# Kernel tuning notes

Hardware: AMD Instinct MI355X
Metric: run time of the kernel (lower is better)

## Reference

```python
import jax, jax.numpy as jnp
import numpy as np

SEQ_LEN = 200
BATCH = 32768
H = 4  # LSTM hidden size


def _lstm_layer(x, Wih, Whh, bih, bhh):
    """PyTorch-semantics LSTM layer. x: [B,T,D] -> [B,T,H]. Gate order i,f,g,o."""
    # precompute input contribution for all timesteps: [B,T,4H]
    xg = jnp.einsum('btd,gd->btg', x, Wih) + bih + bhh

    def step(carry, xt):
        h, c = carry
        g = xt + h @ Whh.T  # [B,4H]
        i, f, gg, o = jnp.split(g, 4, axis=-1)
        c = jax.nn.sigmoid(f) * c + jax.nn.sigmoid(i) * jnp.tanh(gg)
        h = jax.nn.sigmoid(o) * jnp.tanh(c)
        return (h, c), h

    B = x.shape[0]
    z = jnp.zeros((B, Whh.shape[1]), x.dtype)
    _, hs = jax.lax.scan(step, (z, z), jnp.swapaxes(xg, 0, 1))  # [T,B,H]
    return jnp.swapaxes(hs, 0, 1)


def _lstm2(x, Wih0, Whh0, bih0, bhh0, Wih1, Whh1, bih1, bhh1):
    h = _lstm_layer(x, Wih0, Whh0, bih0, bhh0)
    return _lstm_layer(h, Wih1, Whh1, bih1, bhh1)


def setup_inputs() -> dict:
    key = jax.random.key(0)
    ks = iter(jax.random.split(key, 64))
    def p(shape, s=0.1):
        return jax.random.normal(next(ks), shape, jnp.float32) * s
    d = {"x": jax.random.normal(next(ks), (BATCH, 2, SEQ_LEN), jnp.float32)}
    for r in ("r0", "r1"):
        d[f"{r}_Wih0"] = p((4 * H, 1)); d[f"{r}_Whh0"] = p((4 * H, H))
        d[f"{r}_bih0"] = p((4 * H,));  d[f"{r}_bhh0"] = p((4 * H,))
        d[f"{r}_Wih1"] = p((4 * H, H)); d[f"{r}_Whh1"] = p((4 * H, H))
        d[f"{r}_bih1"] = p((4 * H,));  d[f"{r}_bhh1"] = p((4 * H,))
    d["Wp"] = p((40, 2 * SEQ_LEN)); d["bp"] = p((40,))
    d["WH"] = p((128, 4 * SEQ_LEN)); d["bH"] = p((128,))
    d["WL"] = p((128, 4 * SEQ_LEN)); d["bL"] = p((128,))
    d["W1"] = p((80, 256)); d["b1"] = p((80,))
    d["W2"] = p((40, 80)); d["b2"] = p((40,))
    d["W3"] = p((1, 80)); d["b3"] = p((1,))
    return d


def reference(x,
              r0_Wih0, r0_Whh0, r0_bih0, r0_bhh0, r0_Wih1, r0_Whh1, r0_bih1, r0_bhh1,
              r1_Wih0, r1_Whh0, r1_bih0, r1_bhh0, r1_Wih1, r1_Whh1, r1_bih1, r1_bhh1,
              Wp, bp, WH, bH, WL, bL, W1, b1, W2, b2, W3, b3):
    B = x.shape[0]
    x_flat = x.reshape(B, 2 * SEQ_LEN)
    other = x_flat @ Wp.T + bp  # [B,40]

    Hx = x[:, 0, :, None]  # [B,T,1]
    Lx = x[:, 1, :, None]
    Hh = _lstm2(Hx, r0_Wih0, r0_Whh0, r0_bih0, r0_bhh0, r0_Wih1, r0_Whh1, r0_bih1, r0_bhh1)
    Lh = _lstm2(Lx, r1_Wih0, r1_Whh0, r1_bih0, r1_bhh0, r1_Wih1, r1_Whh1, r1_bih1, r1_bhh1)
    Hf = jnp.tanh(Hh.reshape(B, 4 * SEQ_LEN) @ WH.T + bH)  # [B,128]
    Lf = jnp.tanh(Lh.reshape(B, 4 * SEQ_LEN) @ WL.T + bL)
    z = jnp.concatenate([Hf, Lf], axis=1)  # [B,256]
    z = jnp.tanh(z @ W1.T + b1)  # [B,80]
    z = jnp.tanh(z @ W2.T + b2)  # [B,40]
    z = jnp.concatenate([z, other], axis=1)  # [B,80]
    return jax.nn.sigmoid(z @ W3.T + b3)  # [B,1]
```

## Files before the change

### kernel.cpp

```cpp
#include <hip/hip_runtime.h>
#include <hip/hip_bf16.h>

#define BATCH 32768
#define TSEQ 200

typedef __attribute__((ext_vector_type(8))) short short8;
typedef __attribute__((ext_vector_type(4))) float floatx4;
typedef __attribute__((ext_vector_type(2))) float f32x2;

#if __has_builtin(__builtin_amdgcn_exp2f)
__device__ __forceinline__ float EXP2(float x) { return __builtin_amdgcn_exp2f(x); }
#else
__device__ __forceinline__ float EXP2(float x) {
    float r; asm("v_exp_f32 %0, %1" : "=v"(r) : "v"(x)); return r;
}
#endif

__device__ __forceinline__ float fast_sigmoid(float x) {
    return __builtin_amdgcn_rcpf(1.0f + EXP2(-1.4426950408889634f * x));
}
__device__ __forceinline__ float fast_tanh(float x) {
    float e = EXP2(2.8853900817779268f * x);
    return 1.0f - 2.0f * __builtin_amdgcn_rcpf(e + 1.0f);
}
__device__ __forceinline__ short f2bfs(float v) {
    __hip_bfloat16 h = __float2bfloat16(v);
    return __builtin_bit_cast(short, h);
}
__device__ __forceinline__ f32x2 splat2(float x) { f32x2 v; v[0] = x; v[1] = x; return v; }
__device__ __forceinline__ f32x2 pkfma(f32x2 a, f32x2 b, f32x2 c) {
    return __builtin_elementwise_fma(a, b, c);
}
template <int K>
__device__ __forceinline__ float qb(float v) {
    int i = __builtin_bit_cast(int, v);
    int r = __builtin_amdgcn_update_dpp(i, i, K * 0x55, 0xf, 0xf, false);
    return __builtin_bit_cast(float, r);
}
__device__ __forceinline__ void rcp4(float d0, float d1, float d2, float d3,
                                     float& i0, float& i1, float& i2, float& i3) {
    float p01 = d0 * d1, p23 = d2 * d3;
    float r = __builtin_amdgcn_rcpf(p01 * p23);
    float r01 = r * p23, r23 = r * p01;
    i0 = r01 * d1; i1 = r01 * d0; i2 = r23 * d3; i3 = r23 * d2;
}
__device__ __forceinline__ void async16(void* lds, const void* g) {
    __builtin_amdgcn_global_load_lds(
        (const __attribute__((address_space(1))) unsigned int*)g,
        (__attribute__((address_space(3))) unsigned int*)lds, 16, 0, 0);
}

#define S_SIG (-1.4426950408889634f)
#define S_TANH (2.8853900817779268f)

#define WS_HH  0
#define WS_WHB 104857600
#define WS_WLB (WS_WHB + 204800)
#define WS_W1B (WS_WLB + 204800)
#define WS_W2B (WS_W1B + 40960)
#define WS_U   (WS_W2B + 9216)
#define WS_OT  (WS_U + 1616)
#define WS_Z   (WS_OT + 262144)

struct LW { const float* p[16]; };

__global__ __launch_bounds__(256) void k_prep(
    const float* __restrict__ WH, const float* __restrict__ WL,
    const float* __restrict__ W1, const float* __restrict__ W2,
    const float* __restrict__ W3, const float* __restrict__ Wp,
    const float* __restrict__ bp, const float* __restrict__ b3,
    __hip_bfloat16* __restrict__ WHbf, __hip_bfloat16* __restrict__ WLbf,
    __hip_bfloat16* __restrict__ W1bf, __hip_bfloat16* __restrict__ W2bf,
    float* __restrict__ u)
{
    int gid = blockIdx.x * 256 + threadIdx.x;
    int n = gid / 800, k = gid - n * 800;
    int t = k >> 2, q = k & 3;
    int kp = (t >> 2) * 16 + q * 4 + (t & 3);
    int dst = n * 800 + kp;
    WHbf[dst] = __float2bfloat16(WH[gid]);
    WLbf[dst] = __float2bfloat16(WL[gid]);
    if (gid < 20480) W1bf[gid] = __float2bfloat16(W1[gid]);
    if (gid < 4608) {
        int rr = gid / 96, cc = gid - rr * 96;
        float v = (rr < 40 && cc < 80) ? W2[rr * 80 + cc] : 0.0f;
        W2bf[gid] = __float2bfloat16(v);
    }
    if (gid < 400) {
        float a = 0.f;
        for (int j = 0; j < 40; ++j) a = fmaf(W3[40 + j], Wp[j * 400 + gid], a);
        u[gid] = a;
    } else if (gid == 400) {
        float a = b3[0];
        for (int j = 0; j < 40; ++j) a = fmaf(W3[40 + j], bp[j], a);
        u[400] = a;
    }
}

__global__ __launch_bounds__(256, 4) void k_lstm(
    const float* __restrict__ x, LW w, const float* __restrict__ u,
    __hip_bfloat16* __restrict__ hh, float* __restrict__ otherp)
{
    int gid = blockIdx.x * 256 + threadIdx.x;
    int q = gid & 3;
    int group = gid >> 2;
    int b = group & (BATCH - 1);
    int r = group >> 15;

    const float* Wih0 = w.p[r * 8 + 0];
    const float* Whh0 = w.p[r * 8 + 1];
    const float* bih0 = w.p[r * 8 + 2];
    const float* bhh0 = w.p[r * 8 + 3];
    const float* Wih1 = w.p[r * 8 + 4];
    const float* Whh1 = w.p[r * 8 + 5];
    const float* bih1 = w.p[r * 8 + 6];
    const float* bhh1 = w.p[r * 8 + 7];

    f32x2 wx0p[2], bb0p[2], bb1p[2], whh0p[2][4], wih1p[2][4], whh1p[2][4];
#pragma unroll
    for (int p = 0; p < 2; ++p) {
#pragma unroll
        for (int c = 0; c < 2; ++c) {
            int G = 2 * p + c;
            int j = 4 * G + q;
            float sc = (G == 2) ? S_TANH : S_SIG;
            wx0p[p][c] = Wih0[j] * sc;
            bb0p[p][c] = (bih0[j] + bhh0[j]) * sc;
            bb1p[p][c] = (bih1[j] + bhh1[j]) * sc;
#pragma unroll
            for (int k = 0; k < 4; ++k) {
                whh0p[p][k][c] = Whh0[j * 4 + k] * sc;
                wih1p[p][k][c] = Wih1[j * 4 + k] * sc;
                whh1p[p][k][c] = Whh1[j * 4 + k] * sc;
            }
        }
    }

    const float* xp = x + ((size_t)b * 2 + r) * TSEQ;
    const float* up = u + r * TSEQ;
    __hip_bfloat16* hp = hh + ((size_t)r * BATCH + b) * 800 + q * 4;

    float h0 = 0.f, c0 = 0.f, h1 = 0.f, c1 = 0.f, accO = 0.f;

    for (int tb = 0; tb < TSEQ; tb += 4) {
        float4 xv = *(const float4*)(xp + tb);
        float4 uv = *(const float4*)(up + tb);
        float xa[4] = {xv.x, xv.y, xv.z, xv.w};
        float ua[4] = {uv.x, uv.y, uv.z, uv.w};
        float hb[4];
#pragma unroll
        for (int j = 0; j < 4; ++j) {
            float xt = xa[j];
            accO = fmaf(xt, ua[j], accO);

            float a0 = qb<0>(h0), a1 = qb<1>(h0), a2 = qb<2>(h0), a3 = qb<3>(h0);
            f32x2 g0 = pkfma(splat2(xt), wx0p[0], bb0p[0]);
            f32x2 g1 = pkfma(splat2(xt), wx0p[1], bb0p[1]);
            g0 = pkfma(whh0p[0][0], splat2(a0), g0); g1 = pkfma(whh0p[1][0], splat2(a0), g1);
            g0 = pkfma(whh0p[0][1], splat2(a1), g0); g1 = pkfma(whh0p[1][1], splat2(a1), g1);
            g0 = pkfma(whh0p[0][2], splat2(a2), g0); g1 = pkfma(whh0p[1][2], splat2(a2), g1);
            g0 = pkfma(whh0p[0][3], splat2(a3), g0); g1 = pkfma(whh0p[1][3], splat2(a3), g1);
            float di = 1.0f + EXP2(g0[0]);
            float df = 1.0f + EXP2(g0[1]);
            float dt = 1.0f + EXP2(g1[0]);
            float dn = 1.0f + EXP2(g1[1]);
            float ig, fg, it_, og;
            rcp4(di, df, dt, dn, ig, fg, it_, og);
            float tg = fmaf(-2.0f, it_, 1.0f);
            c0 = fmaf(fg, c0, ig * tg);
            float dc0 = 1.0f + EXP2(S_TANH * c0);
            float th0 = fmaf(-2.0f, __builtin_amdgcn_rcpf(dc0), 1.0f);
            h0 = og * th0;

            float p0 = qb<0>(h0), p1 = qb<1>(h0), p2 = qb<2>(h0), p3 = qb<3>(h0);
            float q0 = qb<0>(h1), q1 = qb<1>(h1), q2 = qb<2>(h1), q3 = qb<3>(h1);
            g0 = bb1p[0]; g1 = bb1p[1];
            g0 = pkfma(wih1p[0][0], splat2(p0), g0); g1 = pkfma(wih1p[1][0], splat2(p0), g1);
            g0 = pkfma(wih1p[0][1], splat2(p1), g0); g1 = pkfma(wih1p[1][1], splat2(p1), g1);
            g0 = pkfma(wih1p[0][2], splat2(p2), g0); g1 = pkfma(wih1p[1][2], splat2(p2), g1);
            g0 = pkfma(wih1p[0][3], splat2(p3), g0); g1 = pkfma(wih1p[1][3], splat2(p3), g1);
            g0 = pkfma(whh1p[0][0], splat2(q0), g0); g1 = pkfma(whh1p[1][0], splat2(q0), g1);
            g0 = pkfma(whh1p[0][1], splat2(q1), g0); g1 = pkfma(whh1p[1][1], splat2(q1), g1);
            g0 = pkfma(whh1p[0][2], splat2(q2), g0); g1 = pkfma(whh1p[1][2], splat2(q2), g1);
            g0 = pkfma(whh1p[0][3], splat2(q3), g0); g1 = pkfma(whh1p[1][3], splat2(q3), g1);
            di = 1.0f + EXP2(g0[0]);
            df = 1.0f + EXP2(g0[1]);
            dt = 1.0f + EXP2(g1[0]);
            dn = 1.0f + EXP2(g1[1]);
            rcp4(di, df, dt, dn, ig, fg, it_, og);
            tg = fmaf(-2.0f, it_, 1.0f);
            c1 = fmaf(fg, c1, ig * tg);
            float dc1 = 1.0f + EXP2(S_TANH * c1);
            float th1 = fmaf(-2.0f, __builtin_amdgcn_rcpf(dc1), 1.0f);
            h1 = og * th1;
            hb[j] = h1;
        }
        ushort4 pk;
        pk.x = (unsigned short)f2bfs(hb[0]);
        pk.y = (unsigned short)f2bfs(hb[1]);
        pk.z = (unsigned short)f2bfs(hb[2]);
        pk.w = (unsigned short)f2bfs(hb[3]);
        *(ushort4*)(hp + tb * 4) = pk;
    }
    if (q == 0) otherp[(size_t)r * BATCH + b] = accO;
}

__global__ __launch_bounds__(256) void k_gemm(
    const __hip_bfloat16* __restrict__ hh,
    const __hip_bfloat16* __restrict__ WHbf, const __hip_bfloat16* __restrict__ WLbf,
    const float* __restrict__ bH, const float* __restrict__ bL,
    __hip_bfloat16* __restrict__ zws)
{
    __shared__ __hip_bfloat16 As[2][128 * 32];
    __shared__ __hip_bfloat16 Bs[2][128 * 32];
    int tid = threadIdx.x;
    int f = blockIdx.y;
    int m0 = blockIdx.x * 128;
    const __hip_bfloat16* A = hh + (size_t)f * BATCH * 800 + (size_t)m0 * 800;
    const __hip_bfloat16* Wb = f ? WLbf : WHbf;
    const float* bias = f ? bL : bH;

    int wv = tid >> 6, lane = tid & 63, l15 = lane & 15, quad = lane >> 4;
    const __hip_bfloat16* ga = A + (size_t)(tid >> 2) * 800 + (tid & 3) * 8;
    const __hip_bfloat16* gb = Wb + (size_t)(tid >> 2) * 800 + (tid & 3) * 8;

    floatx4 acc[2][8] = {};

#define PREFETCH(kc, buf)                                              \
    do {                                                               \
        __hip_bfloat16* la = &As[buf][wv * 512];                       \
        __hip_bfloat16* lb = &Bs[buf][wv * 512];                       \
        async16(la,        ga + (kc) * 32);                            \
        async16(lb,        gb + (kc) * 32);                            \
        async16(la + 2048, ga + 64 * 800 + (kc) * 32);                 \
        async16(lb + 2048, gb + 64 * 800 + (kc) * 32);                 \
    } while (0)

    PREFETCH(0, 0);
    for (int kc = 0; kc < 25; ++kc) {
        __syncthreads();
        if (kc < 24) PREFETCH(kc + 1, (kc + 1) & 1);
        int buf = kc & 1;
        short8 af0 = *(const short8*)(const void*)&As[buf][(wv * 32 + l15) * 32 + quad * 8];
        short8 af1 = *(const short8*)(const void*)&As[buf][(wv * 32 + 16 + l15) * 32 + quad * 8];
#pragma unroll
        for (int nt = 0; nt < 8; ++nt) {
            short8 bfr = *(const short8*)(const void*)&Bs[buf][(nt * 16 + l15) * 32 + quad * 8];
            acc[0][nt] = __builtin_amdgcn_mfma_f32_16x16x32_bf16(af0, bfr, acc[0][nt], 0, 0, 0);
            acc[1][nt] = __builtin_amdgcn_mfma_f32_16x16x32_bf16(af1, bfr, acc[1][nt], 0, 0, 0);
        }
    }
#undef PREFETCH

    float bv[8];
#pragma unroll
    for (int nt = 0; nt < 8; ++nt) bv[nt] = bias[nt * 16 + l15];
#pragma unroll
    for (int mt = 0; mt < 2; ++mt)
#pragma unroll
        for (int nt = 0; nt < 8; ++nt)
#pragma unroll
            for (int rg = 0; rg < 4; ++rg) {
                int row = m0 + wv * 32 + mt * 16 + quad * 4 + rg;
                int col = f * 128 + nt * 16 + l15;
                zws[(size_t)row * 256 + col] =
                    __float2bfloat16(fast_tanh(acc[mt][nt][rg] + bv[nt]));
            }
}

__global__ __launch_bounds__(256) void k_tail(
    const __hip_bfloat16* __restrict__ zws,
    const __hip_bfloat16* __restrict__ W1bf, const __hip_bfloat16* __restrict__ W2bf,
    const float* __restrict__ b1, const float* __restrict__ b2,
    const float* __restrict__ W3, const float* __restrict__ u,
    const float* __restrict__ otherp, float* __restrict__ out)
{
    __shared__ short z1sh[64 * 104];
    __shared__ float z2sh[64 * 49];
    int tid = threadIdx.x;
    int wv = tid >> 6, lane = tid & 63, l15 = lane & 15, quad = lane >> 4;
    int m0 = blockIdx.x * 64;

    for (int i = tid; i < 64 * 24; i += 256) {
        int rr = i / 24, cc = 80 + (i - rr * 24);
        z1sh[rr * 104 + cc] = 0;
    }

    {
        floatx4 acc[5] = {};
#pragma unroll
        for (int kc = 0; kc < 8; ++kc) {
            short8 af = *(const short8*)(const void*)
                (zws + (size_t)(m0 + wv * 16 + l15) * 256 + kc * 32 + quad * 8);
#pragma unroll
            for (int nt = 0; nt < 5; ++nt) {
                short8 bfr = *(const short8*)(const void*)
                    (W1bf + (size_t)(nt * 16 + l15) * 256 + kc * 32 + quad * 8);
                acc[nt] = __builtin_amdgcn_mfma_f32_16x16x32_bf16(af, bfr, acc[nt], 0, 0, 0);
            }
        }
#pragma unroll
        for (int nt = 0; nt < 5; ++nt) {
            int n = nt * 16 + l15;
            float bb = b1[n];
#pragma unroll
            for (int rg = 0; rg < 4; ++rg) {
                int ml = wv * 16 + quad * 4 + rg;
                z1sh[ml * 104 + n] = f2bfs(fast_tanh(acc[nt][rg] + bb));
            }
        }
    }
    __syncthreads();

    {
        floatx4 acc[3] = {};
#pragma unroll
        for (int kc = 0; kc < 3; ++kc) {
            short8 af = *(const short8*)(const void*)
                &z1sh[(wv * 16 + l15) * 104 + kc * 32 + quad * 8];
#pragma unroll
            for (int nt = 0; nt < 3; ++nt) {
                short8 bfr = *(const short8*)(const void*)
                    (W2bf + (size_t)(nt * 16 + l15) * 96 + kc * 32 + quad * 8);
                acc[nt] = __builtin_amdgcn_mfma_f32_16x16x32_bf16(af, bfr, acc[nt], 0, 0, 0);
            }
        }
#pragma unroll
        for (int nt = 0; nt < 3; ++nt) {
            int n = nt * 16 + l15;
            if (n < 40) {
                float bb = b2[n];
#pragma unroll
                for (int rg = 0; rg < 4; ++rg) {
                    int ml = wv * 16 + quad * 4 + rg;
                    z2sh[ml * 49 + n] = fast_tanh(acc[nt][rg] + bb);
                }
            }
        }
    }
    __syncthreads();

    if (tid < 64) {
        int grow = m0 + tid;
        float s = u[400] + otherp[grow] + otherp[BATCH + grow];
        for (int j = 0; j < 40; ++j) s = fmaf(z2sh[tid * 49 + j], W3[j], s);
        out[grow] = fast_sigmoid(s);
    }
}

extern "C" void kernel_launch(void* const* d_in, const int* in_sizes, int n_in,
                              void* d_out, int out_size, void* d_ws, size_t ws_size,
                              hipStream_t stream)
{
    const float* x = (const float*)d_in[0];
    LW w;
    for (int i = 0; i < 16; ++i) w.p[i] = (const float*)d_in[1 + i];
    const float* Wp = (const float*)d_in[17];
    const float* bp = (const float*)d_in[18];
    const float* WH = (const float*)d_in[19];
    const float* bH = (const float*)d_in[20];
    const float* WL = (const float*)d_in[21];
    const float* bL = (const float*)d_in[22];
    const float* W1 = (const float*)d_in[23];
    const float* b1 = (const float*)d_in[24];
    const float* W2 = (const float*)d_in[25];
    const float* b2 = (const float*)d_in[26];
    const float* W3 = (const float*)d_in[27];
    const float* b3 = (const float*)d_in[28];

    char* ws = (char*)d_ws;
    __hip_bfloat16* hh   = (__hip_bfloat16*)(ws + WS_HH);
    __hip_bfloat16* WHbf = (__hip_bfloat16*)(ws + WS_WHB);
    __hip_bfloat16* WLbf = (__hip_bfloat16*)(ws + WS_WLB);
    __hip_bfloat16* W1bf = (__hip_bfloat16*)(ws + WS_W1B);
    __hip_bfloat16* W2bf = (__hip_bfloat16*)(ws + WS_W2B);
    float* u      = (float*)(ws + WS_U);
    float* otherp = (float*)(ws + WS_OT);
    __hip_bfloat16* zws = (__hip_bfloat16*)(ws + WS_Z);
    float* out = (float*)d_out;

    k_prep<<<400, 256, 0, stream>>>(WH, WL, W1, W2, W3, Wp, bp, b3,
                                    WHbf, WLbf, W1bf, W2bf, u);
    k_lstm<<<1024, 256, 0, stream>>>(x, w, u, hh, otherp);
    k_gemm<<<dim3(256, 2), 256, 0, stream>>>(hh, WHbf, WLbf, bH, bL, zws);
    k_tail<<<512, 256, 0, stream>>>(zws, W1bf, W2bf, b1, b2, W3, u, otherp, out);
}
```

Baseline: 349.6 us.

## Fuse head GEMM into tail MLP kernel and pin LSTM weights in registers

The separate WH/WL projection GEMM kernel is merged into the tail kernel. Each 64-row block now computes both 128-wide feature halves into shared memory and runs the W1/W2/W3 MLP directly, with no round trip of the z activations through global memory and one fewer launch. The cost is a smaller M tile per block, so weight tiles are reused less and WH/WL are reloaded more often. The LSTM kernel also switches to an explicit waves_per_eu attribute and uses empty asm constraints to keep its weights resident in VGPRs.

Result: no change. 356.1 us (+1.8%).

```diff
diff --git a/kernel.cpp b/kernel.cpp
--- a/kernel.cpp
+++ b/kernel.cpp
@@ -31,6 +31,7 @@
 __device__ __forceinline__ f32x2 pkfma(f32x2 a, f32x2 b, f32x2 c) {
     return __builtin_elementwise_fma(a, b, c);
 }
+__device__ __forceinline__ void pin2(f32x2& v) { asm volatile("" : "+v"(v)); }
 template <int K>
 __device__ __forceinline__ float qb(float v) {
     int i = __builtin_bit_cast(int, v);
@@ -60,7 +61,6 @@
 #define WS_W2B (WS_W1B + 40960)
 #define WS_U   (WS_W2B + 9216)
 #define WS_OT  (WS_U + 1616)
-#define WS_Z   (WS_OT + 262144)
 
 struct LW { const float* p[16]; };
 
@@ -97,7 +97,8 @@
     }
 }
 
-__global__ __launch_bounds__(256, 4) void k_lstm(
+__global__ __launch_bounds__(256)
+__attribute__((amdgpu_waves_per_eu(4, 4))) void k_lstm(
     const float* __restrict__ x, LW w, const float* __restrict__ u,
     __hip_bfloat16* __restrict__ hh, float* __restrict__ otherp)
 {
@@ -133,6 +134,14 @@
                 wih1p[p][k][c] = Wih1[j * 4 + k] * sc;
                 whh1p[p][k][c] = Whh1[j * 4 + k] * sc;
             }
+        }
+    }
+#pragma unroll
+    for (int p = 0; p < 2; ++p) {
+        pin2(wx0p[p]); pin2(bb0p[p]); pin2(bb1p[p]);
+#pragma unroll
+        for (int k = 0; k < 4; ++k) {
+            pin2(whh0p[p][k]); pin2(wih1p[p][k]); pin2(whh1p[p][k]);
         }
     }
 
@@ -205,98 +214,92 @@
     if (q == 0) otherp[(size_t)r * BATCH + b] = accO;
 }
 
-__global__ __launch_bounds__(256) void k_gemm(
+__global__ __launch_bounds__(256) void k_head(
     const __hip_bfloat16* __restrict__ hh,
     const __hip_bfloat16* __restrict__ WHbf, const __hip_bfloat16* __restrict__ WLbf,
     const float* __restrict__ bH, const float* __restrict__ bL,
-    __hip_bfloat16* __restrict__ zws)
-{
-    __shared__ __hip_bfloat16 As[2][128 * 32];
-    __shared__ __hip_bfloat16 Bs[2][128 * 32];
-    int tid = threadIdx.x;
-    int f = blockIdx.y;
-    int m0 = blockIdx.x * 128;
-    const __hip_bfloat16* A = hh + (size_t)f * BATCH * 800 + (size_t)m0 * 800;
-    const __hip_bfloat16* Wb = f ? WLbf : WHbf;
-    const float* bias = f ? bL : bH;
-
-    int wv = tid >> 6, lane = tid & 63, l15 = lane & 15, quad = lane >> 4;
-    const __hip_bfloat16* ga = A + (size_t)(tid >> 2) * 800 + (tid & 3) * 8;
-    const __hip_bfloat16* gb = Wb + (size_t)(tid >> 2) * 800 + (tid & 3) * 8;
-
-    floatx4 acc[2][8] = {};
-
-#define PREFETCH(kc, buf)                                              \
-    do {                                                               \
-        __hip_bfloat16* la = &As[buf][wv * 512];                       \
-        __hip_bfloat16* lb = &Bs[buf][wv * 512];                       \
-        async16(la,        ga + (kc) * 32);                            \
-        async16(lb,        gb + (kc) * 32);                            \
-        async16(la + 2048, ga + 64 * 800 + (kc) * 32);                 \
-        async16(lb + 2048, gb + 64 * 800 + (kc) * 32);                 \
-    } while (0)
-
-    PREFETCH(0, 0);
-    for (int kc = 0; kc < 25; ++kc) {
-        __syncthreads();
-        if (kc < 24) PREFETCH(kc + 1, (kc + 1) & 1);
-        int buf = kc & 1;
-        short8 af0 = *(const short8*)(const void*)&As[buf][(wv * 32 + l15) * 32 + quad * 8];
-        short8 af1 = *(const short8*)(const void*)&As[buf][(wv * 32 + 16 + l15) * 32 + quad * 8];
-#pragma unroll
-        for (int nt = 0; nt < 8; ++nt) {
-            short8 bfr = *(const short8*)(const void*)&Bs[buf][(nt * 16 + l15) * 32 + quad * 8];
-            acc[0][nt] = __builtin_amdgcn_mfma_f32_16x16x32_bf16(af0, bfr, acc[0][nt], 0, 0, 0);
-            acc[1][nt] = __builtin_amdgcn_mfma_f32_16x16x32_bf16(af1, bfr, acc[1][nt], 0, 0, 0);
-        }
-    }
-#undef PREFETCH
-
-    float bv[8];
-#pragma unroll
-    for (int nt = 0; nt < 8; ++nt) bv[nt] = bias[nt * 16 + l15];
-#pragma unroll
-    for (int mt = 0; mt < 2; ++mt)
-#pragma unroll
-        for (int nt = 0; nt < 8; ++nt)
-#pragma unroll
-            for (int rg = 0; rg < 4; ++rg) {
-                int row = m0 + wv * 32 + mt * 16 + quad * 4 + rg;
-                int col = f * 128 + nt * 16 + l15;
-                zws[(size_t)row * 256 + col] =
-                    __float2bfloat16(fast_tanh(acc[mt][nt][rg] + bv[nt]));
-            }
-}
-
-__global__ __launch_bounds__(256) void k_tail(
-    const __hip_bfloat16* __restrict__ zws,
     const __hip_bfloat16* __restrict__ W1bf, const __hip_bfloat16* __restrict__ W2bf,
     const float* __restrict__ b1, const float* __restrict__ b2,
     const float* __restrict__ W3, const float* __restrict__ u,
     const float* __restrict__ otherp, float* __restrict__ out)
 {
-    __shared__ short z1sh[64 * 104];
-    __shared__ float z2sh[64 * 49];
+    __shared__ short zsh[64 * 264];
+    __shared__ __align__(16) char pool[25856];
+    __hip_bfloat16* As = (__hip_bfloat16*)pool;
+    __hip_bfloat16* Bs = (__hip_bfloat16*)(pool + 8192);
+    short* z1sh = (short*)pool;
+    float* z2sh = (float*)(pool + 13312);
+
     int tid = threadIdx.x;
     int wv = tid >> 6, lane = tid & 63, l15 = lane & 15, quad = lane >> 4;
     int m0 = blockIdx.x * 64;
 
+    int arow = tid >> 2, aseg = tid & 3;
+
+    floatx4 acc[8];
+
+    for (int f = 0; f < 2; ++f) {
+        const __hip_bfloat16* A = hh + ((size_t)f * BATCH + m0) * 800;
+        const __hip_bfloat16* Wb = f ? WLbf : WHbf;
+        const float* bias = f ? bL : bH;
+        const __hip_bfloat16* ga = A + (size_t)arow * 800 + aseg * 8;
+        const __hip_bfloat16* gb = Wb + (size_t)(arow + wv * 16) * 800 + aseg * 8;
+
+#define PREFETCH(kc, buf)                                               \
+    do {                                                                \
+        async16(&As[(buf) * 2048 + wv * 512], ga + (kc) * 32);          \
+        async16(&Bs[(buf) * 4096 + wv * 1024], gb + (kc) * 32);         \
+        async16(&Bs[(buf) * 4096 + wv * 1024 + 512],                    \
+                gb + 16 * 800 + (kc) * 32);                             \
+    } while (0)
+
+        if (f == 1) __syncthreads();
+#pragma unroll
+        for (int nt = 0; nt < 8; ++nt) acc[nt] = (floatx4){0.f, 0.f, 0.f, 0.f};
+        PREFETCH(0, 0);
+        for (int kc = 0; kc < 25; ++kc) {
+            __syncthreads();
+            if (kc < 24) PREFETCH(kc + 1, (kc + 1) & 1);
+            int buf = kc & 1;
+            short8 af = *(const short8*)(const void*)
+                &As[buf * 2048 + (wv * 16 + l15) * 32 + quad * 8];
+#pragma unroll
+            for (int nt = 0; nt < 8; ++nt) {
+                short8 bfr = *(const short8*)(const void*)
+                    &Bs[buf * 4096 + (nt * 16 + l15) * 32 + quad * 8];
+                acc[nt] = __builtin_amdgcn_mfma_f32_16x16x32_bf16(af, bfr, acc[nt], 0, 0, 0);
+            }
+        }
+#undef PREFETCH
+#pragma unroll
+        for (int nt = 0; nt < 8; ++nt) {
+            int n = nt * 16 + l15;
+            float bb = bias[n];
+#pragma unroll
+            for (int rg = 0; rg < 4; ++rg) {
+                int ml = wv * 16 + quad * 4 + rg;
+                zsh[ml * 264 + f * 128 + n] = f2bfs(fast_tanh(acc[nt][rg] + bb));
+            }
+        }
+    }
+    __syncthreads();
+
     for (int i = tid; i < 64 * 24; i += 256) {
         int rr = i / 24, cc = 80 + (i - rr * 24);
         z1sh[rr * 104 + cc] = 0;
     }
 
     {
-        floatx4 acc[5] = {};
+        floatx4 acc1[5] = {};
 #pragma unroll
         for (int kc = 0; kc < 8; ++kc) {
             short8 af = *(const short8*)(const void*)
-                (zws + (size_t)(m0 + wv * 16 + l15) * 256 + kc * 32 + quad * 8);
+                &zsh[(wv * 16 + l15) * 264 + kc * 32 + quad * 8];
 #pragma unroll
             for (int nt = 0; nt < 5; ++nt) {
                 short8 bfr = *(const short8*)(const void*)
                     (W1bf + (size_t)(nt * 16 + l15) * 256 + kc * 32 + quad * 8);
-                acc[nt] = __builtin_amdgcn_mfma_f32_16x16x32_bf16(af, bfr, acc[nt], 0, 0, 0);
+                acc1[nt] = __builtin_amdgcn_mfma_f32_16x16x32_bf16(af, bfr, acc1[nt], 0, 0, 0);
             }
         }
 #pragma unroll
@@ -306,14 +309,14 @@
 #pragma unroll
             for (int rg = 0; rg < 4; ++rg) {
                 int ml = wv * 16 + quad * 4 + rg;
-                z1sh[ml * 104 + n] = f2bfs(fast_tanh(acc[nt][rg] + bb));
+                z1sh[ml * 104 + n] = f2bfs(fast_tanh(acc1[nt][rg] + bb));
             }
         }
     }
     __syncthreads();
 
     {
-        floatx4 acc[3] = {};
+        floatx4 acc2[3] = {};
 #pragma unroll
         for (int kc = 0; kc < 3; ++kc) {
             short8 af = *(const short8*)(const void*)
@@ -322,7 +325,7 @@
             for (int nt = 0; nt < 3; ++nt) {
                 short8 bfr = *(const short8*)(const void*)
                     (W2bf + (size_t)(nt * 16 + l15) * 96 + kc * 32 + quad * 8);
-                acc[nt] = __builtin_amdgcn_mfma_f32_16x16x32_bf16(af, bfr, acc[nt], 0, 0, 0);
+                acc2[nt] = __builtin_amdgcn_mfma_f32_16x16x32_bf16(af, bfr, acc2[nt], 0, 0, 0);
             }
         }
 #pragma unroll
@@ -333,7 +336,7 @@
 #pragma unroll
                 for (int rg = 0; rg < 4; ++rg) {
                     int ml = wv * 16 + quad * 4 + rg;
-                    z2sh[ml * 49 + n] = fast_tanh(acc[nt][rg] + bb);
+                    z2sh[ml * 49 + n] = fast_tanh(acc2[nt][rg] + bb);
                 }
             }
         }
@@ -376,12 +379,11 @@
     __hip_bfloat16* W2bf = (__hip_bfloat16*)(ws + WS_W2B);
     float* u      = (float*)(ws + WS_U);
     float* otherp = (float*)(ws + WS_OT);
-    __hip_bfloat16* zws = (__hip_bfloat16*)(ws + WS_Z);
     float* out = (float*)d_out;
 
     k_prep<<<400, 256, 0, stream>>>(WH, WL, W1, W2, W3, Wp, bp, b3,
                                     WHbf, WLbf, W1bf, W2bf, u);
     k_lstm<<<1024, 256, 0, stream>>>(x, w, u, hh, otherp);
-    k_gemm<<<dim3(256, 2), 256, 0, stream>>>(hh, WHbf, WLbf, bH, bL, zws);
-    k_tail<<<512, 256, 0, stream>>>(zws, W1bf, W2bf, b1, b2, W3, u, otherp, out);
-}
+    k_head<<<512, 256, 0, stream>>>(hh, WHbf, WLbf, bH, bL,
+                                    W1bf, W2bf, b1, b2, W3, u, otherp, out);
+}
```
